# Optimization experiments

Hardware: AMD Instinct MI355X
Metric: run time of the kernel (lower is better)

The kernel has to match this reference:

```python
import jax, jax.numpy as jnp
import numpy as np

N_HEADS = 4
N_NODES = 10000
EMB = 128
N_BATCH = 4096
N_NEAREST = 8
N_SENTINELS = 8


def setup_inputs() -> dict:
    key = jax.random.key(0)
    k1, k2, k3, k4 = jax.random.split(key, 4)
    embeds = jax.random.normal(k1, (N_HEADS, N_NODES, EMB), jnp.float32)
    field = jax.random.uniform(k3, (N_HEADS, N_NODES, EMB), dtype=jnp.float32)
    uncertainty = jnp.ones((1, 1, 1), jnp.float32) * 5.0
    adj = (jax.random.uniform(k4, (N_NODES, N_NODES)) < 0.001).astype(jnp.float32)
    batch_edges = jax.random.randint(k2, (2, N_BATCH), 0, N_NODES)
    return {"embeds": embeds, "field": field, "uncertainty": uncertainty,
            "adj": adj, "batch_edges": batch_edges}


def _knn_samples(embeds, nodes, k):
    # embeds: (h, n, d); nodes: (b,) -> indices of k nearest neighbors, excluding self.
    # Squared L2 distance is monotone in L2 norm, so top-k order matches the
    # original's .norm(dim=3).topk(..., largest=False).
    x = embeds[:, nodes]                                  # (h, b, d)
    x2 = jnp.sum(x * x, axis=-1)[:, :, None]              # (h, b, 1)
    y2 = jnp.sum(embeds * embeds, axis=-1)[:, None, :]    # (h, 1, n)
    d2 = x2 + y2 - 2.0 * jnp.einsum('hbd,hnd->hbn', x, embeds)  # (h, b, n)
    _, idx = jax.lax.top_k(-d2, k + 1)                    # nearest first
    return jax.lax.stop_gradient(idx[:, :, 1:])           # drop self -> (h, b, k)


def reference(embeds, field, uncertainty, adj, batch_edges):
    src, dst = batch_edges[0], batch_edges[1]
    h_idx = jnp.arange(N_HEADS)[:, None, None]

    def build(nodes, nodes_logits, adj_gather):
        samples = _knn_samples(embeds, nodes, N_NEAREST)                 # (h,b,k)
        diff = embeds[:, nodes][:, :, None, :] - embeds[h_idx, samples]  # (h,b,k,d)
        label = uncertainty * (adj_gather(samples) * 2.0 - 1.0)          # (h,b,k)
        g = field[:, nodes_logits]                                        # (h,b,d)
        logits = jnp.einsum('hbkd,hbd->hbk', diff, g) + label
        return logits, diff

    src_logits, src_diff = build(src, dst, lambda s: adj[s, dst[None, :, None]])
    tgt_logits, tgt_diff = build(dst, src, lambda s: adj[src[None, :, None], s])

    logits = jnp.concatenate([src_logits, tgt_logits], axis=2)           # (h,b,2k)
    dist = jnp.linalg.norm(jnp.concatenate([src_diff, tgt_diff], axis=2), axis=3)

    h, b = logits.shape[0], logits.shape[1]
    logits = jnp.concatenate(
        [logits, jnp.zeros((h, b, N_SENTINELS), logits.dtype)], axis=2)
    dist = jnp.concatenate(
        [dist, jnp.ones((h, b, N_SENTINELS), dist.dtype)], axis=2)

    # softmin: softmax(1 - dist)-weighted sum of logits, then mean over heads
    softmin = jnp.sum(logits * jax.nn.softmax(1.0 - dist, axis=2), axis=2)  # (h,b)
    return jax.nn.sigmoid(softmin.mean(axis=0)).reshape(-1)                 # (b,)
```

## Files before the change

### kernel.cpp

```cpp
#include <hip/hip_runtime.h>
#include <math.h>
#include <stdint.h>

#define N_HEADS 4
#define N_NODES 10000
#define NPAD 10112
#define NPG (NPAD / 32)
#define EMB 128
#define N_BATCH 4096
#define NQ (2 * N_BATCH)
#define K 8
#define TQ 32
#define TN 128
#define NTILES (NPAD / TN)
#define PH 2
#define CAP 41

typedef __attribute__((ext_vector_type(8))) __bf16 bf16x8;
typedef __attribute__((ext_vector_type(8))) unsigned short ushortx8;
typedef __attribute__((ext_vector_type(16))) float floatx16;

__device__ __forceinline__ unsigned short f2bf(float x) {
  unsigned u = __float_as_uint(x);
  u += 0x7fff + ((u >> 16) & 1);
  return (unsigned short)(u >> 16);
}
__device__ __forceinline__ float bf2f(unsigned short h) {
  return __uint_as_float(((unsigned)h) << 16);
}
__device__ __forceinline__ uint32_t bfup(float f) {
  uint32_t u = __float_as_uint(f);
  return (f >= 0.f) ? ((u + 0xFFFFu) >> 16) : (u >> 16);
}

__device__ __forceinline__ void insert8(float* bs, int* bi, float s, int node) {
  if (s < bs[K - 1]) {
    #pragma unroll
    for (int k2 = K - 1; k2 >= 0; --k2) {
      if (!(s < bs[k2])) break;
      if (k2 < K - 1) { bs[k2 + 1] = bs[k2]; bi[k2 + 1] = bi[k2]; }
      bs[k2] = s; bi[k2] = node;
    }
  }
}

__device__ __forceinline__ size_t pchunk(int g, int c, int lm) {
  return (size_t)g * 4096 + (size_t)(c >> 1) * 512 + (size_t)(c & 1) * 256 + lm * 8;
}

__global__ __launch_bounds__(256) void prep_kernel(
    const float* __restrict__ E, unsigned short* __restrict__ EhiP,
    unsigned short* __restrict__ EloP, float* __restrict__ y2g) {
  __shared__ float s_p[8][33];
  const int h = blockIdx.y, g = blockIdx.x;
  const int lm = threadIdx.x & 31, c8 = threadIdx.x >> 5;
  const int n = g * 32 + lm;
  float x[16];
  #pragma unroll
  for (int j = 0; j < 16; ++j) x[j] = 0.f;
  if (n < N_NODES) {
    const float* src = E + (size_t)(h * N_NODES + n) * EMB + c8 * 16;
    #pragma unroll
    for (int j = 0; j < 4; ++j) {
      float4 v = *(const float4*)(src + j * 4);
      x[j * 4 + 0] = v.x; x[j * 4 + 1] = v.y; x[j * 4 + 2] = v.z; x[j * 4 + 3] = v.w;
    }
  }
  float part = 0.f;
  ushortx8 hi[2], lo[2];
  #pragma unroll
  for (int j = 0; j < 16; ++j) {
    part += x[j] * x[j];
    unsigned short hv = f2bf(x[j]);
    unsigned short lv = f2bf(x[j] - bf2f(hv));
    hi[j >> 3][j & 7] = hv;
    lo[j >> 3][j & 7] = lv;
  }
  size_t base = (size_t)h * NPG * 4096;
  #pragma unroll
  for (int lh = 0; lh < 2; ++lh) {
    size_t off = base + pchunk(g, c8 * 2 + lh, lm);
    *(ushortx8*)&EhiP[off] = hi[lh];
    *(ushortx8*)&EloP[off] = lo[lh];
  }
  s_p[c8][lm] = part;
  __syncthreads();
  if (threadIdx.x < 32) {
    int nn = g * 32 + threadIdx.x;
    float s = 0.f;
    #pragma unroll
    for (int j = 0; j < 8; ++j) s += s_p[j][threadIdx.x];
    y2g[h * NPAD + nn] = (nn < N_NODES) ? s : 1e30f;
  }
}

__global__ __launch_bounds__(256, 4) void knn_kernel(
    const unsigned short* __restrict__ EhiP, const unsigned short* __restrict__ EloP,
    const float* __restrict__ y2g, const int* __restrict__ be,
    int* __restrict__ samples) {
  __shared__ __align__(16) float s_x[TQ * TN];
  __shared__ __align__(16) unsigned short s_alo[TQ * EMB];
  __shared__ float s_t8S[TQ * 9];
  __shared__ int   s_t8I[TQ * 9];
  __shared__ float s_lsS[TQ * CAP];
  __shared__ int   s_lsI[TQ * CAP];
  __shared__ float s_thr[TQ];
  __shared__ int   s_cnt[TQ];

  const int id = blockIdx.x;
  const int h = (id & 7) >> 1;
  const int qt = ((id >> 3) << 1) | (id & 1);
  const int tid = threadIdx.x;
  const int lane = tid & 63;
  const int w1 = tid >> 6;
  const int lm = lane & 31, lh = lane >> 5;
  const unsigned short* EhiH = EhiP + (size_t)h * NPG * 4096;
  const unsigned short* EloH = EloP + (size_t)h * NPG * 4096;
  const float* y2H = y2g + h * NPAD;

  bf16x8 ahi[8];
  unsigned short* s_xq = (unsigned short*)s_x;
  {
    int r = tid >> 3, cb = (tid & 7) * 2;
    int rx15 = r & 15;
    int q = be[qt * TQ + r];
    int gq = q >> 5, lmq = q & 31;
    const int arx = lm & 15;
    #pragma unroll
    for (int c = 0; c < 2; ++c) {
      int lc = cb + c;
      *(bf16x8*)&s_xq[r * EMB + (lc ^ rx15) * 8] =
          *(const bf16x8*)&EhiH[pchunk(gq, lc, lmq)];
    }
    __syncthreads();
    #pragma unroll
    for (int ks = 0; ks < 8; ++ks)
      ahi[ks] = *(const bf16x8*)&s_xq[lm * EMB + (((ks * 2 + lh) ^ arx)) * 8];
    __syncthreads();
    #pragma unroll
    for (int c = 0; c < 2; ++c) {
      int lc = cb + c;
      *(bf16x8*)&s_alo[r * EMB + (lc ^ rx15) * 8] =
          *(const bf16x8*)&EloH[pchunk(gq, lc, lmq)];
    }
    __syncthreads();
  }

  const int qsel = tid >> 3;
  const int csel = tid & 7;
  const int myq = be[qt * TQ + qsel];
  float bs[K]; int bi[K];
  #pragma unroll
  for (int k2 = 0; k2 < K; ++k2) { bs[k2] = 1e30f; bi[k2] = 0x7fffffff; }
  if (tid < TQ) s_cnt[tid] = 0;

  const int bnode = 32 * w1 + lm;
  const int arx = lm & 15;
  const unsigned short* bhp = EhiH + (size_t)w1 * 4096 + lane * 8;
  const unsigned short* blp = EloH + (size_t)w1 * 4096 + lane * 8;

  #pragma unroll 1
  for (int t = 0; t < PH; ++t) {
    const size_t goff = (size_t)t * 16384;
    float ny = y2H[t * TN + bnode];
    floatx16 acc = {0.f, 0.f, 0.f, 0.f, 0.f, 0.f, 0.f, 0.f,
                    0.f, 0.f, 0.f, 0.f, 0.f, 0.f, 0.f, 0.f};
    #pragma unroll
    for (int ks = 0; ks < 8; ++ks) {
      bf16x8 va = *(const bf16x8*)&s_alo[lm * EMB + (((ks * 2 + lh) ^ arx)) * 8];
      bf16x8 vbh = *(const bf16x8*)(bhp + goff + ks * 512);
      bf16x8 vbl = *(const bf16x8*)(blp + goff + ks * 512);
      acc = __builtin_amdgcn_mfma_f32_32x32x16_bf16(va, vbh, acc, 0, 0, 0);
      acc = __builtin_amdgcn_mfma_f32_32x32x16_bf16(ahi[ks], vbl, acc, 0, 0, 0);
      acc = __builtin_amdgcn_mfma_f32_32x32x16_bf16(ahi[ks], vbh, acc, 0, 0, 0);
    }
    #pragma unroll
    for (int r = 0; r < 16; ++r) {
      int row = (r & 3) + 8 * (r >> 2) + 4 * lh;
      s_x[row * TN + bnode] = fmaf(-2.f, acc[r], ny);
    }
    __syncthreads();
    int nbp = t * TN;
    #pragma unroll
    for (int s = 0; s < 16; ++s) {
      int j = csel * 16 + ((s + qsel) & 15);
      float sc = s_x[qsel * TN + j];
      int node = nbp + j;
      if (node != myq) insert8(bs, bi, sc, node);
    }
    __syncthreads();
  }

  {
    float* scrS = (float*)s_x;
    int*   scrI = (int*)s_x + TQ * 64;
    #pragma unroll
    for (int k2 = 0; k2 < K; ++k2) {
      scrS[tid * 8 + k2] = bs[k2]; scrI[tid * 8 + k2] = bi[k2];
    }
    __syncthreads();
    if (tid < TQ) {
      int q = tid;
      float ts[K]; int ti[K];
      #pragma unroll
      for (int k2 = 0; k2 < K; ++k2) { ts[k2] = 1e30f; ti[k2] = 0x7fffffff; }
      for (int kk = 0; kk < 64; ++kk) {
        int e = (kk + q) & 63;
        insert8(ts, ti, scrS[q * 64 + e], scrI[q * 64 + e]);
      }
      s_thr[q] = ts[K - 1];
      #pragma unroll
      for (int k2 = 0; k2 < K; ++k2) { s_t8S[q * 9 + k2] = ts[k2]; s_t8I[q * 9 + k2] = ti[k2]; }
    }
    __syncthreads();
  }

  uint32_t thrp[8];
  #pragma unroll
  for (int j = 0; j < 8; ++j) {
    int r0 = 2 * j, r1 = 2 * j + 1;
    float t0 = s_thr[(r0 & 3) + 8 * (r0 >> 2) + 4 * lh];
    float t1 = s_thr[(r1 & 3) + 8 * (r1 >> 2) + 4 * lh];
    thrp[j] = bfup(t0) | (bfup(t1) << 16);
  }

  #pragma unroll 1
  for (int t = PH; t < NTILES; ++t) {
    if (t == 4 || t == 8 || t == 16 || t == 32) {
      __syncthreads();
      if (tid < TQ) {
        int q = tid;
        int myqm = be[qt * TQ + q];
        float ts[K]; int ti[K];
        #pragma unroll
        for (int k2 = 0; k2 < K; ++k2) { ts[k2] = s_t8S[q * 9 + k2]; ti[k2] = s_t8I[q * 9 + k2]; }
        int cnt = s_cnt[q]; if (cnt > CAP) cnt = CAP;
        for (int p = 0; p < cnt; ++p) {
          int iv = s_lsI[q * CAP + p];
          if (iv != myqm) insert8(ts, ti, s_lsS[q * CAP + p], iv);
        }
        s_cnt[q] = 0;
        s_thr[q] = ts[K - 1];
        #pragma unroll
        for (int k2 = 0; k2 < K; ++k2) { s_t8S[q * 9 + k2] = ts[k2]; s_t8I[q * 9 + k2] = ti[k2]; }
      }
      __syncthreads();
      #pragma unroll
      for (int j = 0; j < 8; ++j) {
        int r0 = 2 * j, r1 = 2 * j + 1;
        float t0 = s_thr[(r0 & 3) + 8 * (r0 >> 2) + 4 * lh];
        float t1 = s_thr[(r1 & 3) + 8 * (r1 >> 2) + 4 * lh];
        thrp[j] = bfup(t0) | (bfup(t1) << 16);
      }
    }

    const size_t goff = (size_t)t * 16384;
    float ny = y2H[t * TN + bnode];
    floatx16 acc = {0.f, 0.f, 0.f, 0.f, 0.f, 0.f, 0.f, 0.f,
                    0.f, 0.f, 0.f, 0.f, 0.f, 0.f, 0.f, 0.f};
    #pragma unroll
    for (int ks = 0; ks < 8; ++ks) {
      bf16x8 va = *(const bf16x8*)&s_alo[lm * EMB + (((ks * 2 + lh) ^ arx)) * 8];
      bf16x8 vbh = *(const bf16x8*)(bhp + goff + ks * 512);
      bf16x8 vbl = *(const bf16x8*)(blp + goff + ks * 512);
      acc = __builtin_amdgcn_mfma_f32_32x32x16_bf16(va, vbh, acc, 0, 0, 0);
      acc = __builtin_amdgcn_mfma_f32_32x32x16_bf16(ahi[ks], vbl, acc, 0, 0, 0);
      acc = __builtin_amdgcn_mfma_f32_32x32x16_bf16(ahi[ks], vbh, acc, 0, 0, 0);
    }
    const int node = t * TN + bnode;
    #pragma unroll
    for (int r = 0; r < 16; ++r) {
      float sc = fmaf(-2.f, acc[r], ny);
      float th = (r & 1) ? __uint_as_float(thrp[r >> 1] & 0xFFFF0000u)
                         : __uint_as_float(thrp[r >> 1] << 16);
      if (sc < th) {
        int q = (r & 3) + 8 * (r >> 2) + 4 * lh;
        int p = atomicAdd(&s_cnt[q], 1);
        if (p < CAP) { s_lsS[q * CAP + p] = sc; s_lsI[q * CAP + p] = node; }
      }
    }
  }

  __syncthreads();
  if (tid < TQ) {
    int q = tid;
    int myqm = be[qt * TQ + q];
    float ts[K]; int ti[K];
    #pragma unroll
    for (int k2 = 0; k2 < K; ++k2) { ts[k2] = s_t8S[q * 9 + k2]; ti[k2] = s_t8I[q * 9 + k2]; }
    int cnt = s_cnt[q]; if (cnt > CAP) cnt = CAP;
    for (int p = 0; p < cnt; ++p) {
      int iv = s_lsI[q * CAP + p];
      if (iv != myqm) insert8(ts, ti, s_lsS[q * CAP + p], iv);
    }
    size_t base = ((size_t)h * NQ + qt * TQ + q) * K;
    #pragma unroll
    for (int k2 = 0; k2 < K; ++k2) samples[base + k2] = ti[k2];
  }
}

__global__ __launch_bounds__(256) void predict_kernel(
    const float* __restrict__ E, const float* __restrict__ F,
    const float* __restrict__ unc, const float* __restrict__ adj,
    const int* __restrict__ be, const int* __restrict__ samples,
    float* __restrict__ out) {
  int b = blockIdx.x;
  int h = threadIdx.x >> 6;
  int lane = threadIdx.x & 63;
  __shared__ float smv[N_HEADS];

  int srcb = be[b];
  int dstb = be[N_BATCH + b];
  const float* Eh = E + (size_t)h * N_NODES * EMB;
  const float* Fh = F + (size_t)h * N_NODES * EMB;
  float2 es = *(const float2*)(Eh + (size_t)srcb * EMB + 2 * lane);
  float2 ed = *(const float2*)(Eh + (size_t)dstb * EMB + 2 * lane);
  float2 fs = *(const float2*)(Fh + (size_t)srcb * EMB + 2 * lane);
  float2 fd = *(const float2*)(Fh + (size_t)dstb * EMB + 2 * lane);
  float u = unc[0];

  float logit[16], dist[16];
  #pragma unroll
  for (int j = 0; j < 16; ++j) {
    bool isrc = (j < 8);
    int qrow = isrc ? b : (N_BATCH + b);
    int s = samples[((size_t)h * NQ + qrow) * K + (j & 7)];
    float2 ev = *(const float2*)(Eh + (size_t)s * EMB + 2 * lane);
    float2 bb = isrc ? es : ed;
    float2 g = isrc ? fd : fs;
    float dx = bb.x - ev.x, dy = bb.y - ev.y;
    float dot = dx * g.x + dy * g.y;
    float nrm = dx * dx + dy * dy;
    #pragma unroll
    for (int o = 32; o > 0; o >>= 1) {
      dot += __shfl_xor(dot, o);
      nrm += __shfl_xor(nrm, o);
    }
    float a = isrc ? adj[(size_t)s * N_NODES + dstb]
                   : adj[(size_t)srcb * N_NODES + s];
    logit[j] = dot + u * (2.0f * a - 1.0f);
    dist[j] = sqrtf(nrm);
  }

  float m = 0.0f;
  #pragma unroll
  for (int j = 0; j < 16; ++j) m = fmaxf(m, 1.0f - dist[j]);
  float Z = 8.0f * expf(-m);
  float num = 0.0f;
  #pragma unroll
  for (int j = 0; j < 16; ++j) {
    float e = expf(1.0f - dist[j] - m);
    Z += e;
    num += logit[j] * e;
  }
  if (lane == 0) smv[h] = num / Z;
  __syncthreads();
  if (threadIdx.x == 0) {
    float t = 0.25f * (smv[0] + smv[1] + smv[2] + smv[3]);
    out[b] = 1.0f / (1.0f + expf(-t));
  }
}

extern "C" void kernel_launch(void* const* d_in, const int* in_sizes, int n_in,
                              void* d_out, int out_size, void* d_ws,
                              size_t ws_size, hipStream_t stream) {
  const float* E = (const float*)d_in[0];
  const float* F = (const float*)d_in[1];
  const float* U = (const float*)d_in[2];
  const float* A = (const float*)d_in[3];
  const int* be = (const int*)d_in[4];
  float* out = (float*)d_out;

  char* w = (char*)d_ws;
  unsigned short* EhiP = (unsigned short*)(w);
  unsigned short* EloP = (unsigned short*)(w + 10354688);
  float* y2g = (float*)(w + 20709376);
  int* samples = (int*)(w + 20871424);

  prep_kernel<<<dim3(NPG, N_HEADS), 256, 0, stream>>>(E, EhiP, EloP, y2g);
  knn_kernel<<<dim3((NQ / TQ) * N_HEADS), 256, 0, stream>>>(EhiP, EloP, y2g, be, samples);
  predict_kernel<<<dim3(N_BATCH), 256, 0, stream>>>(E, F, U, A, be, samples, out);
}
```

Before: 797.2 us.

## Use single bf16 screening pass with fp32 rescoring of windowed candidates

Replaces the three-MFMA hi/lo split-bf16 distance computation with a single bf16 MFMA per tile. To keep the selection correct, it keeps every candidate within a fixed margin of the current 8th-best score and rescores those candidates in fp32 from the original embeddings before the final top-8 merge. This cuts MFMA work and the global/LDS traffic for the lo halves to about a third. In exchange the candidate lists grow and there is an extra fp32 gather and rescoring phase. Correctness depends on the bf16 error staying under the window and on candidates not overflowing CAP.

Result: faster. 777.2 us (-2.5%).

```diff
diff --git a/kernel.cpp b/kernel.cpp
--- a/kernel.cpp
+++ b/kernel.cpp
@@ -15,6 +15,7 @@
 #define NTILES (NPAD / TN)
 #define PH 2
 #define CAP 41
+#define WIN 0.5f
 
 typedef __attribute__((ext_vector_type(8))) __bf16 bf16x8;
 typedef __attribute__((ext_vector_type(8))) unsigned short ushortx8;
@@ -25,13 +26,6 @@
   u += 0x7fff + ((u >> 16) & 1);
   return (unsigned short)(u >> 16);
 }
-__device__ __forceinline__ float bf2f(unsigned short h) {
-  return __uint_as_float(((unsigned)h) << 16);
-}
-__device__ __forceinline__ uint32_t bfup(float f) {
-  uint32_t u = __float_as_uint(f);
-  return (f >= 0.f) ? ((u + 0xFFFFu) >> 16) : (u >> 16);
-}
 
 __device__ __forceinline__ void insert8(float* bs, int* bi, float s, int node) {
   if (s < bs[K - 1]) {
@@ -50,7 +44,7 @@
 
 __global__ __launch_bounds__(256) void prep_kernel(
     const float* __restrict__ E, unsigned short* __restrict__ EhiP,
-    unsigned short* __restrict__ EloP, float* __restrict__ y2g) {
+    float* __restrict__ y2g) {
   __shared__ float s_p[8][33];
   const int h = blockIdx.y, g = blockIdx.x;
   const int lm = threadIdx.x & 31, c8 = threadIdx.x >> 5;
@@ -67,22 +61,16 @@
     }
   }
   float part = 0.f;
-  ushortx8 hi[2], lo[2];
+  ushortx8 hi[2];
   #pragma unroll
   for (int j = 0; j < 16; ++j) {
     part += x[j] * x[j];
-    unsigned short hv = f2bf(x[j]);
-    unsigned short lv = f2bf(x[j] - bf2f(hv));
-    hi[j >> 3][j & 7] = hv;
-    lo[j >> 3][j & 7] = lv;
+    hi[j >> 3][j & 7] = f2bf(x[j]);
   }
   size_t base = (size_t)h * NPG * 4096;
   #pragma unroll
-  for (int lh = 0; lh < 2; ++lh) {
-    size_t off = base + pchunk(g, c8 * 2 + lh, lm);
-    *(ushortx8*)&EhiP[off] = hi[lh];
-    *(ushortx8*)&EloP[off] = lo[lh];
-  }
+  for (int lh = 0; lh < 2; ++lh)
+    *(ushortx8*)&EhiP[base + pchunk(g, c8 * 2 + lh, lm)] = hi[lh];
   s_p[c8][lm] = part;
   __syncthreads();
   if (threadIdx.x < 32) {
@@ -95,11 +83,10 @@
 }
 
 __global__ __launch_bounds__(256, 4) void knn_kernel(
-    const unsigned short* __restrict__ EhiP, const unsigned short* __restrict__ EloP,
-    const float* __restrict__ y2g, const int* __restrict__ be,
+    const unsigned short* __restrict__ EhiP, const float* __restrict__ y2g,
+    const float* __restrict__ Ef, const int* __restrict__ be,
     int* __restrict__ samples) {
   __shared__ __align__(16) float s_x[TQ * TN];
-  __shared__ __align__(16) unsigned short s_alo[TQ * EMB];
   __shared__ float s_t8S[TQ * 9];
   __shared__ int   s_t8I[TQ * 9];
   __shared__ float s_lsS[TQ * CAP];
@@ -115,8 +102,8 @@
   const int w1 = tid >> 6;
   const int lm = lane & 31, lh = lane >> 5;
   const unsigned short* EhiH = EhiP + (size_t)h * NPG * 4096;
-  const unsigned short* EloH = EloP + (size_t)h * NPG * 4096;
   const float* y2H = y2g + h * NPAD;
+  const float* EH = Ef + (size_t)h * N_NODES * EMB;
 
   bf16x8 ahi[8];
   unsigned short* s_xq = (unsigned short*)s_x;
@@ -125,7 +112,6 @@
     int rx15 = r & 15;
     int q = be[qt * TQ + r];
     int gq = q >> 5, lmq = q & 31;
-    const int arx = lm & 15;
     #pragma unroll
     for (int c = 0; c < 2; ++c) {
       int lc = cb + c;
@@ -133,16 +119,10 @@
           *(const bf16x8*)&EhiH[pchunk(gq, lc, lmq)];
     }
     __syncthreads();
+    const int arx = lm & 15;
     #pragma unroll
     for (int ks = 0; ks < 8; ++ks)
       ahi[ks] = *(const bf16x8*)&s_xq[lm * EMB + (((ks * 2 + lh) ^ arx)) * 8];
-    __syncthreads();
-    #pragma unroll
-    for (int c = 0; c < 2; ++c) {
-      int lc = cb + c;
-      *(bf16x8*)&s_alo[r * EMB + (lc ^ rx15) * 8] =
-          *(const bf16x8*)&EloH[pchunk(gq, lc, lmq)];
-    }
     __syncthreads();
   }
 
@@ -155,9 +135,7 @@
   if (tid < TQ) s_cnt[tid] = 0;
 
   const int bnode = 32 * w1 + lm;
-  const int arx = lm & 15;
   const unsigned short* bhp = EhiH + (size_t)w1 * 4096 + lane * 8;
-  const unsigned short* blp = EloH + (size_t)w1 * 4096 + lane * 8;
 
   #pragma unroll 1
   for (int t = 0; t < PH; ++t) {
@@ -167,11 +145,7 @@
                     0.f, 0.f, 0.f, 0.f, 0.f, 0.f, 0.f, 0.f};
     #pragma unroll
     for (int ks = 0; ks < 8; ++ks) {
-      bf16x8 va = *(const bf16x8*)&s_alo[lm * EMB + (((ks * 2 + lh) ^ arx)) * 8];
       bf16x8 vbh = *(const bf16x8*)(bhp + goff + ks * 512);
-      bf16x8 vbl = *(const bf16x8*)(blp + goff + ks * 512);
-      acc = __builtin_amdgcn_mfma_f32_32x32x16_bf16(va, vbh, acc, 0, 0, 0);
-      acc = __builtin_amdgcn_mfma_f32_32x32x16_bf16(ahi[ks], vbl, acc, 0, 0, 0);
       acc = __builtin_amdgcn_mfma_f32_32x32x16_bf16(ahi[ks], vbh, acc, 0, 0, 0);
     }
     #pragma unroll
@@ -208,21 +182,29 @@
         int e = (kk + q) & 63;
         insert8(ts, ti, scrS[q * 64 + e], scrI[q * 64 + e]);
       }
-      s_thr[q] = ts[K - 1];
+      float thr = ts[K - 1], win = thr + WIN;
+      int nc = 0;
+      for (int kk = 0; kk < 64; ++kk) {
+        int e = (kk + q) & 63;
+        float sv = scrS[q * 64 + e]; int iv = scrI[q * 64 + e];
+        if (sv <= win && nc < CAP) {
+          bool dup = false;
+          #pragma unroll
+          for (int j = 0; j < K; ++j) dup = dup || (ti[j] == iv);
+          if (!dup) { s_lsS[q * CAP + nc] = sv; s_lsI[q * CAP + nc] = iv; ++nc; }
+        }
+      }
+      s_cnt[q] = nc;
+      s_thr[q] = win;
       #pragma unroll
       for (int k2 = 0; k2 < K; ++k2) { s_t8S[q * 9 + k2] = ts[k2]; s_t8I[q * 9 + k2] = ti[k2]; }
     }
     __syncthreads();
   }
 
-  uint32_t thrp[8];
-  #pragma unroll
-  for (int j = 0; j < 8; ++j) {
-    int r0 = 2 * j, r1 = 2 * j + 1;
-    float t0 = s_thr[(r0 & 3) + 8 * (r0 >> 2) + 4 * lh];
-    float t1 = s_thr[(r1 & 3) + 8 * (r1 >> 2) + 4 * lh];
-    thrp[j] = bfup(t0) | (bfup(t1) << 16);
-  }
+  float thrf[16];
+  #pragma unroll
+  for (int r = 0; r < 16; ++r) thrf[r] = s_thr[(r & 3) + 8 * (r >> 2) + 4 * lh];
 
   #pragma unroll 1
   for (int t = PH; t < NTILES; ++t) {
@@ -239,19 +221,35 @@
           int iv = s_lsI[q * CAP + p];
           if (iv != myqm) insert8(ts, ti, s_lsS[q * CAP + p], iv);
         }
-        s_cnt[q] = 0;
-        s_thr[q] = ts[K - 1];
+        float thr = ts[K - 1], win = thr + WIN;
+        int nc = 0;
+        for (int p = 0; p < cnt; ++p) {
+          float sv = s_lsS[q * CAP + p]; int iv = s_lsI[q * CAP + p];
+          if (sv <= win && iv != myqm) {
+            bool dup = false;
+            #pragma unroll
+            for (int j = 0; j < K; ++j) dup = dup || (ti[j] == iv);
+            if (!dup && nc < CAP) { s_lsS[q * CAP + nc] = sv; s_lsI[q * CAP + nc] = iv; ++nc; }
+          }
+        }
+        #pragma unroll
+        for (int k2 = 0; k2 < K; ++k2) {
+          float sv = s_t8S[q * 9 + k2]; int iv = s_t8I[q * 9 + k2];
+          if (sv <= win && iv != myqm && nc < CAP) {
+            bool dup = false;
+            #pragma unroll
+            for (int j = 0; j < K; ++j) dup = dup || (ti[j] == iv);
+            if (!dup) { s_lsS[q * CAP + nc] = sv; s_lsI[q * CAP + nc] = iv; ++nc; }
+          }
+        }
+        s_cnt[q] = nc;
+        s_thr[q] = win;
         #pragma unroll
         for (int k2 = 0; k2 < K; ++k2) { s_t8S[q * 9 + k2] = ts[k2]; s_t8I[q * 9 + k2] = ti[k2]; }
       }
       __syncthreads();
       #pragma unroll
-      for (int j = 0; j < 8; ++j) {
-        int r0 = 2 * j, r1 = 2 * j + 1;
-        float t0 = s_thr[(r0 & 3) + 8 * (r0 >> 2) + 4 * lh];
-        float t1 = s_thr[(r1 & 3) + 8 * (r1 >> 2) + 4 * lh];
-        thrp[j] = bfup(t0) | (bfup(t1) << 16);
-      }
+      for (int r = 0; r < 16; ++r) thrf[r] = s_thr[(r & 3) + 8 * (r >> 2) + 4 * lh];
     }
 
     const size_t goff = (size_t)t * 16384;
@@ -260,20 +258,14 @@
                     0.f, 0.f, 0.f, 0.f, 0.f, 0.f, 0.f, 0.f};
     #pragma unroll
     for (int ks = 0; ks < 8; ++ks) {
-      bf16x8 va = *(const bf16x8*)&s_alo[lm * EMB + (((ks * 2 + lh) ^ arx)) * 8];
       bf16x8 vbh = *(const bf16x8*)(bhp + goff + ks * 512);
-      bf16x8 vbl = *(const bf16x8*)(blp + goff + ks * 512);
-      acc = __builtin_amdgcn_mfma_f32_32x32x16_bf16(va, vbh, acc, 0, 0, 0);
-      acc = __builtin_amdgcn_mfma_f32_32x32x16_bf16(ahi[ks], vbl, acc, 0, 0, 0);
       acc = __builtin_amdgcn_mfma_f32_32x32x16_bf16(ahi[ks], vbh, acc, 0, 0, 0);
     }
     const int node = t * TN + bnode;
     #pragma unroll
     for (int r = 0; r < 16; ++r) {
       float sc = fmaf(-2.f, acc[r], ny);
-      float th = (r & 1) ? __uint_as_float(thrp[r >> 1] & 0xFFFF0000u)
-                         : __uint_as_float(thrp[r >> 1] << 16);
-      if (sc < th) {
+      if (sc < thrf[r]) {
         int q = (r & 3) + 8 * (r >> 2) + 4 * lh;
         int p = atomicAdd(&s_cnt[q], 1);
         if (p < CAP) { s_lsS[q * CAP + p] = sc; s_lsI[q * CAP + p] = node; }
@@ -281,13 +273,47 @@
     }
   }
 
+  __syncthreads();
+  {
+    int q = tid >> 3, k = tid & 7;
+    int qn = be[qt * TQ + q];
+    const float4* Eq = (const float4*)(EH + (size_t)qn * EMB);
+    int iv = s_t8I[q * 9 + k];
+    if (iv < N_NODES) {
+      const float4* En = (const float4*)(EH + (size_t)iv * EMB);
+      float d0 = 0.f, d1 = 0.f, d2 = 0.f, d3 = 0.f;
+      #pragma unroll
+      for (int d = 0; d < 32; ++d) {
+        float4 a = Eq[d], b = En[d];
+        d0 += a.x * b.x; d1 += a.y * b.y; d2 += a.z * b.z; d3 += a.w * b.w;
+      }
+      s_t8S[q * 9 + k] = y2H[iv] - 2.f * ((d0 + d1) + (d2 + d3));
+    }
+    int cnt = s_cnt[q]; if (cnt > CAP) cnt = CAP;
+    for (int p = k; p < cnt; p += 8) {
+      int jv = s_lsI[q * CAP + p];
+      if (jv < N_NODES && jv != qn) {
+        const float4* En = (const float4*)(EH + (size_t)jv * EMB);
+        float d0 = 0.f, d1 = 0.f, d2 = 0.f, d3 = 0.f;
+        #pragma unroll
+        for (int d = 0; d < 32; ++d) {
+          float4 a = Eq[d], b = En[d];
+          d0 += a.x * b.x; d1 += a.y * b.y; d2 += a.z * b.z; d3 += a.w * b.w;
+        }
+        s_lsS[q * CAP + p] = y2H[jv] - 2.f * ((d0 + d1) + (d2 + d3));
+      }
+    }
+  }
   __syncthreads();
   if (tid < TQ) {
     int q = tid;
     int myqm = be[qt * TQ + q];
     float ts[K]; int ti[K];
     #pragma unroll
-    for (int k2 = 0; k2 < K; ++k2) { ts[k2] = s_t8S[q * 9 + k2]; ti[k2] = s_t8I[q * 9 + k2]; }
+    for (int k2 = 0; k2 < K; ++k2) { ts[k2] = 1e30f; ti[k2] = 0x7fffffff; }
+    #pragma unroll
+    for (int k2 = 0; k2 < K; ++k2)
+      insert8(ts, ti, s_t8S[q * 9 + k2], s_t8I[q * 9 + k2]);
     int cnt = s_cnt[q]; if (cnt > CAP) cnt = CAP;
     for (int p = 0; p < cnt; ++p) {
       int iv = s_lsI[q * CAP + p];
@@ -373,11 +399,10 @@
 
   char* w = (char*)d_ws;
   unsigned short* EhiP = (unsigned short*)(w);
-  unsigned short* EloP = (unsigned short*)(w + 10354688);
-  float* y2g = (float*)(w + 20709376);
-  int* samples = (int*)(w + 20871424);
-
-  prep_kernel<<<dim3(NPG, N_HEADS), 256, 0, stream>>>(E, EhiP, EloP, y2g);
-  knn_kernel<<<dim3((NQ / TQ) * N_HEADS), 256, 0, stream>>>(EhiP, EloP, y2g, be, samples);
+  float* y2g = (float*)(w + 10354688);
+  int* samples = (int*)(w + 10516736);
+
+  prep_kernel<<<dim3(NPG, N_HEADS), 256, 0, stream>>>(E, EhiP, y2g);
+  knn_kernel<<<dim3((NQ / TQ) * N_HEADS), 256, 0, stream>>>(EhiP, y2g, E, be, samples);
   predict_kernel<<<dim3(N_BATCH), 256, 0, stream>>>(E, F, U, A, be, samples, out);
 }
```
